# Performance work log

Measured on AMD Instinct MI355X. Metric: run time of the kernel, lower is better.

## Reference

```python
import jax, jax.numpy as jnp
import numpy as np

N = 50000   # nodes
E = 800000  # edges
F = 128     # feat_dim
LN_EPS = 1e-5


def setup_inputs() -> dict:
    key = jax.random.key(0)
    ks = jax.random.split(key, 16)

    def lin(k, fan_in, shape):
        # roughly kaiming-uniform-like scale; exact init is irrelevant for correctness
        return jax.random.normal(k, shape, jnp.float32) * (1.0 / np.sqrt(fan_in))

    inp = {
        "x": jax.random.normal(ks[0], (N, F), jnp.float32),
        "pos": jax.random.normal(ks[1], (N, 3), jnp.float32),
        "edge_index": jax.random.randint(ks[2], (2, E), 0, N, jnp.int64),
        # edge_mlp: Linear(2F+1 -> F), SiLU, Linear(F -> F)
        "ew1": lin(ks[3], 2 * F + 1, (2 * F + 1, F)),
        "eb1": jnp.zeros((F,), jnp.float32),
        "ew2": lin(ks[4], F, (F, F)),
        "eb2": jnp.zeros((F,), jnp.float32),
        # node_mlp: Linear(F -> F), SiLU, Linear(F -> F)
        "nw1": lin(ks[5], F, (F, F)),
        "nb1": jnp.zeros((F,), jnp.float32),
        "nw2": lin(ks[6], F, (F, F)),
        "nb2": jnp.zeros((F,), jnp.float32),
        # coord_mlp: Linear(F -> 1), Tanh
        "cw": lin(ks[7], F, (F, 1)),
        "cb": jnp.zeros((1,), jnp.float32),
        # LayerNorm(F)
        "gamma": jnp.ones((F,), jnp.float32),
        "beta": jnp.zeros((F,), jnp.float32),
    }
    return inp


def reference(x, pos, edge_index, ew1, eb1, ew2, eb2, nw1, nb1, nw2, nb2, cw, cb, gamma, beta):
    row, col = edge_index[0], edge_index[1]

    diff = pos[row] - pos[col]                              # [E, 3]
    dist2 = jnp.sum(diff * diff, axis=1, keepdims=True)     # [E, 1]
    edge_feat = jnp.concatenate([x[row], x[col], dist2], axis=1)  # [E, 2F+1]

    # edge MLP (dropout p=0 -> identity in eval)
    msg = jax.nn.silu(edge_feat @ ew1 + eb1) @ ew2 + eb2    # [E, F]

    # scatter-add messages to source nodes
    agg = jax.ops.segment_sum(msg, row, num_segments=N)     # [N, F]

    # node MLP + residual + LayerNorm
    upd = jax.nn.silu(agg @ nw1 + nb1) @ nw2 + nb2          # [N, F]
    pre = x + upd
    mean = jnp.mean(pre, axis=-1, keepdims=True)
    var = jnp.mean(jnp.square(pre - mean), axis=-1, keepdims=True)
    x_out = gamma * (pre - mean) * jax.lax.rsqrt(var + LN_EPS) + beta

    # coordinate update
    scale = jnp.tanh(msg @ cw + cb)                         # [E, 1]
    delta = jax.ops.segment_sum(scale * diff, row, num_segments=N)  # [N, 3]
    pos_out = pos + delta
    return (x_out, pos_out)
```

## Files before the change

### kernel.cpp

```cpp
#include <hip/hip_runtime.h>
#include <math.h>

#define NN 50000
#define EE 800000
#define FF 128

constexpr float LN_EPS = 1e-5f;
constexpr int NC = (NN + 255) / 256;

typedef float  f32x4  __attribute__((ext_vector_type(4)));
typedef short  s16x8  __attribute__((ext_vector_type(8)));
typedef unsigned short u16x4 __attribute__((ext_vector_type(4)));

__device__ __forceinline__ float silu_f(float v) {
    return v / (1.f + __expf(-v));
}

__device__ __forceinline__ unsigned short f2bf(float f) {
    union { float f; unsigned u; } cv; cv.f = f;
    unsigned u = cv.u;
    u += 0x7fffu + ((u >> 16) & 1u);
    return (unsigned short)(u >> 16);
}

__device__ __forceinline__ float bf2f(unsigned short u) {
    union { unsigned u; float f; } cv; cv.u = ((unsigned)u) << 16;
    return cv.f;
}

__global__ __launch_bounds__(256) void convert_x_kernel(
    const float* __restrict__ x, unsigned short* __restrict__ xb)
{
    int i = (blockIdx.x * 256 + threadIdx.x) * 8;
    float4 a = *(const float4*)&x[i];
    float4 b = *(const float4*)&x[i + 4];
    s16x8 o;
    o[0] = (short)f2bf(a.x); o[1] = (short)f2bf(a.y);
    o[2] = (short)f2bf(a.z); o[3] = (short)f2bf(a.w);
    o[4] = (short)f2bf(b.x); o[5] = (short)f2bf(b.y);
    o[6] = (short)f2bf(b.z); o[7] = (short)f2bf(b.w);
    *(s16x8*)&xb[i] = o;
}

__global__ __launch_bounds__(256) void transpose_w_kernel(
    const float* __restrict__ ew1, const float* __restrict__ ew2,
    const float* __restrict__ nw1, const float* __restrict__ nw2,
    unsigned short* __restrict__ ew1T, unsigned short* __restrict__ ew2T,
    unsigned short* __restrict__ nw1T, unsigned short* __restrict__ nw2T)
{
    int o = blockIdx.x * 256 + threadIdx.x;
    if (o < 32768) {
        int n = o >> 8, k = o & 255;
        ew1T[o] = f2bf(ew1[k * FF + n]);
    } else if (o < 49152) {
        int o2 = o - 32768; int n = o2 >> 7, k = o2 & 127;
        ew2T[o2] = f2bf(ew2[k * FF + n]);
    } else if (o < 65536) {
        int o2 = o - 49152; int n = o2 >> 7, k = o2 & 127;
        nw1T[o2] = f2bf(nw1[k * FF + n]);
    } else {
        int o2 = o - 65536; int n = o2 >> 7, k = o2 & 127;
        nw2T[o2] = f2bf(nw2[k * FF + n]);
    }
}

__global__ __launch_bounds__(256) void hist_kernel(
    const int* __restrict__ ei, int* __restrict__ cnt)
{
    int e = blockIdx.x * 256 + threadIdx.x;
    if (e < EE) atomicAdd(&cnt[ei[e]], 1);
}

__global__ __launch_bounds__(256) void chunk_sum_kernel(
    const int* __restrict__ cnt, int* __restrict__ chunkSum)
{
    __shared__ int s[256];
    int t = threadIdx.x;
    int idx = blockIdx.x * 256 + t;
    s[t] = (idx < NN) ? cnt[idx] : 0;
    __syncthreads();
    for (int off = 128; off > 0; off >>= 1) {
        if (t < off) s[t] += s[t + off];
        __syncthreads();
    }
    if (t == 0) chunkSum[blockIdx.x] = s[0];
}

__global__ __launch_bounds__(256) void scan_chunks_kernel(
    const int* __restrict__ chunkSum, int* __restrict__ chunkOff)
{
    __shared__ int s[256];
    int t = threadIdx.x;
    int v = (t < NC) ? chunkSum[t] : 0;
    s[t] = v;
    __syncthreads();
    for (int off = 1; off < 256; off <<= 1) {
        int u = (t >= off) ? s[t - off] : 0;
        __syncthreads();
        s[t] += u;
        __syncthreads();
    }
    if (t < NC) chunkOff[t] = s[t] - v;
}

__global__ __launch_bounds__(256) void scan_kernel(
    const int* __restrict__ cnt, const int* __restrict__ chunkOff,
    int* __restrict__ offs, int* __restrict__ rowStart)
{
    __shared__ int s[256];
    int t = threadIdx.x;
    int idx = blockIdx.x * 256 + t;
    int v = (idx < NN) ? cnt[idx] : 0;
    s[t] = v;
    __syncthreads();
    for (int off = 1; off < 256; off <<= 1) {
        int u = (t >= off) ? s[t - off] : 0;
        __syncthreads();
        s[t] += u;
        __syncthreads();
    }
    if (idx < NN) {
        int st = chunkOff[blockIdx.x] + s[t] - v;
        offs[idx] = st;
        rowStart[idx] = st;
    }
}

__global__ __launch_bounds__(256) void scatter_idx_kernel(
    const int* __restrict__ ei, int* __restrict__ offs,
    int* __restrict__ sRow, int* __restrict__ sCol)
{
    int e = blockIdx.x * 256 + threadIdx.x;
    if (e < EE) {
        int r = ei[e], c = ei[EE + e];
        int p = atomicAdd(&offs[r], 1);
        sRow[p] = r;
        sCol[p] = c;
    }
}

constexpr int EPB   = 64;
constexpr int NTILE = EE / EPB;
constexpr int XAS   = 264;
constexpr int H1S   = 136;

__global__ __launch_bounds__(512, 4) void edgeA_kernel(
    const unsigned short* __restrict__ xb, const float* __restrict__ pos,
    const int* __restrict__ sRow, const int* __restrict__ sCol,
    const unsigned short* __restrict__ ew1T, const float* __restrict__ ew1,
    const float* __restrict__ eb1,
    const unsigned short* __restrict__ ew2T, const float* __restrict__ eb2,
    const float* __restrict__ cw,  const float* __restrict__ cb,
    float* __restrict__ agg, float* __restrict__ sSg)
{
    __shared__ float dist2S[EPB];
    __shared__ int   rowS  [EPB];
    __shared__ float sPart[8][EPB];
    __shared__ __align__(16) unsigned short xa  [EPB * XAS];
    __shared__ __align__(16) unsigned short h1  [EPB * H1S];
    __shared__ __align__(16) unsigned short msgL[EPB * H1S];

    const int t   = threadIdx.x;
    const int w   = t >> 6;
    const int l   = t & 63;
    const int l15 = l & 15;
    const int q8  = l >> 4;
    const int n   = w * 16 + l15;

    s16x8 B1[8], B2[4];
    #pragma unroll
    for (int ko = 0; ko < 8; ++ko)
        B1[ko] = *(const s16x8*)(ew1T + (size_t)n * 256 + ko * 32 + q8 * 8);
    #pragma unroll
    for (int ko = 0; ko < 4; ++ko)
        B2[ko] = *(const s16x8*)(ew2T + (size_t)n * 128 + ko * 32 + q8 * 8);
    const float w256 = ew1[256 * FF + n];
    const float b1   = eb1[n];
    const float b2   = eb2[n];
    const float cwc  = cw[n];
    const float cb0  = cb[0];

    const int q   = t & 31;
    const int eB  = t >> 5;
    const int ksel = (q & 15) * 8;
    const int* idxBase = (q < 16) ? sRow : sCol;

    int   nidx[4];
    s16x8 ag[4];
    {
        int e0 = blockIdx.x * EPB;
        #pragma unroll
        for (int i = 0; i < 4; ++i) nidx[i] = idxBase[e0 + eB + 16 * i];
        #pragma unroll
        for (int i = 0; i < 4; ++i) ag[i] = *(const s16x8*)(xb + (size_t)nidx[i] * FF + ksel);
    }

    for (int tile = blockIdx.x; tile < NTILE; tile += gridDim.x) {
        const int e0 = tile * EPB;

        #pragma unroll
        for (int i = 0; i < 4; ++i)
            *(s16x8*)(xa + (eB + 16 * i) * XAS + q * 8) = ag[i];
        if (t < EPB) {
            int r = sRow[e0 + t];
            int c = sCol[e0 + t];
            rowS[t] = r;
            float dx = pos[r*3+0] - pos[c*3+0];
            float dy = pos[r*3+1] - pos[c*3+1];
            float dz = pos[r*3+2] - pos[c*3+2];
            dist2S[t] = dx*dx + dy*dy + dz*dz;
        }
        __syncthreads();

        {
            int tn  = tile + gridDim.x;
            int e0n = (tn < NTILE) ? tn * EPB : 0;
            #pragma unroll
            for (int i = 0; i < 4; ++i) nidx[i] = idxBase[e0n + eB + 16 * i];
            #pragma unroll
            for (int i = 0; i < 4; ++i) ag[i] = *(const s16x8*)(xb + (size_t)nidx[i] * FF + ksel);
        }

        f32x4 acc[4] = {};
        #pragma unroll
        for (int mt = 0; mt < 4; ++mt) {
            const unsigned short* ar = xa + (mt * 16 + l15) * XAS + q8 * 8;
            #pragma unroll
            for (int ko = 0; ko < 8; ++ko) {
                s16x8 a = *(const s16x8*)(ar + ko * 32);
                acc[mt] = __builtin_amdgcn_mfma_f32_16x16x32_bf16(a, B1[ko], acc[mt], 0, 0, 0);
            }
        }

        #pragma unroll
        for (int mt = 0; mt < 4; ++mt) {
            #pragma unroll
            for (int r = 0; r < 4; ++r) {
                int e = mt * 16 + q8 * 4 + r;
                float v = acc[mt][r] + dist2S[e] * w256 + b1;
                h1[e * H1S + n] = f2bf(silu_f(v));
            }
        }
        __syncthreads();

        f32x4 acc2[4] = {};
        #pragma unroll
        for (int mt = 0; mt < 4; ++mt) {
            const unsigned short* hr = h1 + (mt * 16 + l15) * H1S + q8 * 8;
            #pragma unroll
            for (int ko = 0; ko < 4; ++ko) {
                s16x8 a = *(const s16x8*)(hr + ko * 32);
                acc2[mt] = __builtin_amdgcn_mfma_f32_16x16x32_bf16(a, B2[ko], acc2[mt], 0, 0, 0);
            }
        }

        #pragma unroll
        for (int mt = 0; mt < 4; ++mt) {
            #pragma unroll
            for (int r = 0; r < 4; ++r) {
                float m = acc2[mt][r] + b2;
                float p = m * cwc;
                p += __shfl_xor(p, 1);
                p += __shfl_xor(p, 2);
                p += __shfl_xor(p, 4);
                p += __shfl_xor(p, 8);
                int e = mt * 16 + q8 * 4 + r;
                if (l15 == 0) sPart[w][e] = p;
                msgL[e * H1S + n] = f2bf(m);
            }
        }
        __syncthreads();

        if (t < EPB) {
            float p = 0.f;
            #pragma unroll
            for (int ww = 0; ww < 8; ++ww) p += sPart[ww][t];
            sSg[e0 + t] = tanhf(p + cb0);
        }

        {
            int c    = t & 127;
            int s    = t >> 7;
            int base = s * 16;
            float a  = 0.f;
            int cur  = rowS[base];
            #pragma unroll
            for (int k = 0; k < 16; ++k) {
                int e = base + k;
                int r = rowS[e];
                if (r != cur) {
                    atomicAdd(&agg[(size_t)cur * FF + c], a);
                    a = 0.f; cur = r;
                }
                a += bf2f(msgL[e * H1S + c]);
            }
            atomicAdd(&agg[(size_t)cur * FF + c], a);
        }
        __syncthreads();
    }
}

constexpr int NPB = 16;
constexpr int ABS = 136;

__global__ __launch_bounds__(512) void nodeB_kernel(
    const float* __restrict__ x, const float* __restrict__ pos,
    const float* __restrict__ agg, const float* __restrict__ sSg,
    const int* __restrict__ sCol, const int* __restrict__ rowStart,
    const unsigned short* __restrict__ nw1T, const float* __restrict__ nb1,
    const unsigned short* __restrict__ nw2T, const float* __restrict__ nb2,
    const float* __restrict__ gamma, const float* __restrict__ beta,
    float* __restrict__ xout, float* __restrict__ posout)
{
    __shared__ __align__(16) unsigned short aB [NPB * ABS];
    __shared__ __align__(16) unsigned short h1B[NPB * ABS];
    __shared__ float sRedS[8][NPB];
    __shared__ float sRedQ[8][NPB];
    __shared__ float sPosP[NPB][3][4];

    const int t   = threadIdx.x;
    const int w   = t >> 6;
    const int l   = t & 63;
    const int l15 = l & 15;
    const int q8  = l >> 4;
    const int n0  = blockIdx.x * NPB;
    const int n   = w * 16 + l15;

    {
        int idx = t * 4;
        int e = idx >> 7, c = idx & 127;
        float4 v = *(const float4*)&agg[(size_t)(n0 + e) * FF + c];
        u16x4 o;
        o[0] = f2bf(v.x); o[1] = f2bf(v.y); o[2] = f2bf(v.z); o[3] = f2bf(v.w);
        *(u16x4*)(aB + e * ABS + c) = o;
    }

    if (t < NPB * 12) {
        int e   = t / 12;
        int rem = t - e * 12;
        int d   = rem % 3;
        int ch  = rem / 3;
        int nn  = n0 + e;
        int p0  = rowStart[nn];
        int p1  = (nn == NN - 1) ? EE : rowStart[nn + 1];
        float pn = pos[nn * 3 + d];
        float sum = 0.f;
        for (int p = p0 + ch; p < p1; p += 4) {
            int c = sCol[p];
            sum += sSg[p] * (pn - pos[c * 3 + d]);
        }
        sPosP[e][d][ch] = sum;
    }
    __syncthreads();

    if (t < NPB * 3) {
        int e = t / 3, d = t % 3;
        int nn = n0 + e;
        posout[nn * 3 + d] = pos[nn * 3 + d]
            + sPosP[e][d][0] + sPosP[e][d][1] + sPosP[e][d][2] + sPosP[e][d][3];
    }

    f32x4 acc = {};
    {
        const unsigned short* ar = aB + l15 * ABS + q8 * 8;
        #pragma unroll
        for (int ko = 0; ko < 4; ++ko) {
            s16x8 a = *(const s16x8*)(ar + ko * 32);
            s16x8 b = *(const s16x8*)(nw1T + (size_t)n * 128 + ko * 32 + q8 * 8);
            acc = __builtin_amdgcn_mfma_f32_16x16x32_bf16(a, b, acc, 0, 0, 0);
        }
    }
    {
        float bb = nb1[n];
        #pragma unroll
        for (int r = 0; r < 4; ++r) {
            int e = q8 * 4 + r;
            h1B[e * ABS + n] = f2bf(silu_f(acc[r] + bb));
        }
    }
    __syncthreads();

    f32x4 acc2 = {};
    {
        const unsigned short* hr = h1B + l15 * ABS + q8 * 8;
        #pragma unroll
        for (int ko = 0; ko < 4; ++ko) {
            s16x8 a = *(const s16x8*)(hr + ko * 32);
            s16x8 b = *(const s16x8*)(nw2T + (size_t)n * 128 + ko * 32 + q8 * 8);
            acc2 = __builtin_amdgcn_mfma_f32_16x16x32_bf16(a, b, acc2, 0, 0, 0);
        }
    }

    float pre[4];
    {
        float bb = nb2[n];
        #pragma unroll
        for (int r = 0; r < 4; ++r) {
            int e = q8 * 4 + r;
            pre[r] = x[(size_t)(n0 + e) * FF + n] + acc2[r] + bb;
        }
    }
    #pragma unroll
    for (int r = 0; r < 4; ++r) {
        float s = pre[r], sq = pre[r] * pre[r];
        s += __shfl_xor(s, 1);  sq += __shfl_xor(sq, 1);
        s += __shfl_xor(s, 2);  sq += __shfl_xor(sq, 2);
        s += __shfl_xor(s, 4);  sq += __shfl_xor(sq, 4);
        s += __shfl_xor(s, 8);  sq += __shfl_xor(sq, 8);
        if (l15 == 0) {
            int e = q8 * 4 + r;
            sRedS[w][e] = s;
            sRedQ[w][e] = sq;
        }
    }
    __syncthreads();

    {
        float g = gamma[n], bt = beta[n];
        #pragma unroll
        for (int r = 0; r < 4; ++r) {
            int e = q8 * 4 + r;
            float S = 0.f, Q = 0.f;
            #pragma unroll
            for (int ww = 0; ww < 8; ++ww) { S += sRedS[ww][e]; Q += sRedQ[ww][e]; }
            float mean = S * (1.f / FF);
            float var  = Q * (1.f / FF) - mean * mean;
            xout[(size_t)(n0 + e) * FF + n] =
                g * (pre[r] - mean) * rsqrtf(var + LN_EPS) + bt;
        }
    }
}

extern "C" void kernel_launch(void* const* d_in, const int* in_sizes, int n_in,
                              void* d_out, int out_size, void* d_ws, size_t ws_size,
                              hipStream_t stream) {
    const float* x    = (const float*)d_in[0];
    const float* pos  = (const float*)d_in[1];
    const int*   ei   = (const int*)  d_in[2];
    const float* ew1  = (const float*)d_in[3];
    const float* eb1  = (const float*)d_in[4];
    const float* ew2  = (const float*)d_in[5];
    const float* eb2  = (const float*)d_in[6];
    const float* nw1  = (const float*)d_in[7];
    const float* nb1  = (const float*)d_in[8];
    const float* nw2  = (const float*)d_in[9];
    const float* nb2  = (const float*)d_in[10];
    const float* cw   = (const float*)d_in[11];
    const float* cb   = (const float*)d_in[12];
    const float* gam  = (const float*)d_in[13];
    const float* bet  = (const float*)d_in[14];

    float* out    = (float*)d_out;
    float* xout   = out;
    float* posout = out + (size_t)NN * FF;

    auto align256 = [](size_t v) { return (v + 255) & ~(size_t)255; };
    char* ws = (char*)d_ws;

    size_t CNT_B   = align256((size_t)NN * 4);
    size_t OFFS_B  = align256((size_t)NN * 4);
    size_t RST_B   = align256((size_t)NN * 4);
    size_t CHNK_B  = align256((size_t)NC * 4 * 2);
    size_t SROW_B  = align256((size_t)EE * 4);
    size_t XB_B    = align256((size_t)NN * FF * 2);
    size_t EW1T_B  = align256((size_t)128 * 256 * 2);
    size_t WT_B    = align256((size_t)128 * 128 * 2);
    size_t AGG_B   = align256((size_t)NN * FF * 4);

    size_t o = 0;
    int* cnt       = (int*)(ws + o);  o += CNT_B;
    int* offs      = (int*)(ws + o);  o += OFFS_B;
    int* rowStart  = (int*)(ws + o);  o += RST_B;
    int* chunkSum  = (int*)(ws + o);
    int* chunkOff  = chunkSum + NC;   o += CHNK_B;
    int* sRow      = (int*)(ws + o);  o += SROW_B;
    int* sCol      = (int*)(ws + o);  o += SROW_B;
    unsigned short* xb   = (unsigned short*)(ws + o);  o += XB_B;
    unsigned short* ew1T = (unsigned short*)(ws + o);  o += EW1T_B;
    unsigned short* ew2T = (unsigned short*)(ws + o);  o += WT_B;
    unsigned short* nw1T = (unsigned short*)(ws + o);  o += WT_B;
    unsigned short* nw2T = (unsigned short*)(ws + o);  o += WT_B;
    float*          agg  = (float*)(ws + o);           o += AGG_B;
    float*          sSg  = (float*)(ws + o);

    hipMemsetAsync(cnt, 0, CNT_B, stream);
    hipMemsetAsync(agg, 0, (size_t)NN * FF * 4, stream);

    convert_x_kernel<<<(NN * FF / 8) / 256, 256, 0, stream>>>(x, xb);
    transpose_w_kernel<<<(32768 + 3 * 16384) / 256, 256, 0, stream>>>(
        ew1, ew2, nw1, nw2, ew1T, ew2T, nw1T, nw2T);

    hist_kernel<<<(EE + 255) / 256, 256, 0, stream>>>(ei, cnt);
    chunk_sum_kernel<<<NC, 256, 0, stream>>>(cnt, chunkSum);
    scan_chunks_kernel<<<1, 256, 0, stream>>>(chunkSum, chunkOff);
    scan_kernel<<<NC, 256, 0, stream>>>(cnt, chunkOff, offs, rowStart);
    scatter_idx_kernel<<<(EE + 255) / 256, 256, 0, stream>>>(ei, offs, sRow, sCol);

    edgeA_kernel<<<2048, 512, 0, stream>>>(
        xb, pos, sRow, sCol, ew1T, ew1, eb1, ew2T, eb2, cw, cb, agg, sSg);

    nodeB_kernel<<<NN / NPB, 512, 0, stream>>>(
        x, pos, agg, sSg, sCol, rowStart,
        nw1T, nb1, nw2T, nb2, gam, bet, xout, posout);
}
```

Before: 503.1 us.

## Alias msg buffer onto xa, raise edge occupancy, parallelize coordinate reductions

The edge kernel reuses the xa shared buffer for bf16 messages instead of a separate msgL array. This cuts LDS per block, and the launch-bounds hint rises from 4 to 6 blocks per CU. The tanh coordinate-scale reduction now uses all threads with a transposed partial array and shuffles. The scatter now has each wave handle 8 edges with two channels per lane using 32-bit LDS loads. In the node kernel, the per-node position delta now uses 32 lanes per node with xyz together and a shuffle reduction, replacing 12 threads per node and an LDS stage. The higher occupancy target may squeeze registers, and aliasing xa assumes xa is dead by the time messages are written.

```diff
diff --git a/kernel.cpp b/kernel.cpp
--- a/kernel.cpp
+++ b/kernel.cpp
@@ -144,7 +144,7 @@
 constexpr int XAS   = 264;
 constexpr int H1S   = 136;
 
-__global__ __launch_bounds__(512, 4) void edgeA_kernel(
+__global__ __launch_bounds__(512, 6) void edgeA_kernel(
     const unsigned short* __restrict__ xb, const float* __restrict__ pos,
     const int* __restrict__ sRow, const int* __restrict__ sCol,
     const unsigned short* __restrict__ ew1T, const float* __restrict__ ew1,
@@ -155,10 +155,10 @@
 {
     __shared__ float dist2S[EPB];
     __shared__ int   rowS  [EPB];
-    __shared__ float sPart[8][EPB];
+    __shared__ float sPartT[EPB][8];
     __shared__ __align__(16) unsigned short xa  [EPB * XAS];
     __shared__ __align__(16) unsigned short h1  [EPB * H1S];
-    __shared__ __align__(16) unsigned short msgL[EPB * H1S];
+    unsigned short* msgL = xa;
 
     const int t   = threadIdx.x;
     const int w   = t >> 6;
@@ -265,36 +265,42 @@
                 p += __shfl_xor(p, 4);
                 p += __shfl_xor(p, 8);
                 int e = mt * 16 + q8 * 4 + r;
-                if (l15 == 0) sPart[w][e] = p;
+                if (l15 == 0) sPartT[e][w] = p;
                 msgL[e * H1S + n] = f2bf(m);
             }
         }
         __syncthreads();
 
-        if (t < EPB) {
-            float p = 0.f;
-            #pragma unroll
-            for (int ww = 0; ww < 8; ++ww) p += sPart[ww][t];
-            sSg[e0 + t] = tanhf(p + cb0);
-        }
-
         {
-            int c    = t & 127;
-            int s    = t >> 7;
-            int base = s * 16;
-            float a  = 0.f;
+            int e  = t >> 3;
+            int ww = t & 7;
+            float p = sPartT[e][ww];
+            p += __shfl_xor(p, 1);
+            p += __shfl_xor(p, 2);
+            p += __shfl_xor(p, 4);
+            if (ww == 0) sSg[e0 + e] = tanhf(p + cb0);
+        }
+
+        {
+            int c2   = l * 2;
+            int base = w * 8;
+            float a0 = 0.f, a1 = 0.f;
             int cur  = rowS[base];
             #pragma unroll
-            for (int k = 0; k < 16; ++k) {
+            for (int k = 0; k < 8; ++k) {
                 int e = base + k;
                 int r = rowS[e];
                 if (r != cur) {
-                    atomicAdd(&agg[(size_t)cur * FF + c], a);
-                    a = 0.f; cur = r;
+                    atomicAdd(&agg[(size_t)cur * FF + c2],     a0);
+                    atomicAdd(&agg[(size_t)cur * FF + c2 + 1], a1);
+                    a0 = 0.f; a1 = 0.f; cur = r;
                 }
-                a += bf2f(msgL[e * H1S + c]);
+                unsigned v = *(const unsigned*)(msgL + e * H1S + c2);
+                a0 += bf2f((unsigned short)(v & 0xffffu));
+                a1 += bf2f((unsigned short)(v >> 16));
             }
-            atomicAdd(&agg[(size_t)cur * FF + c], a);
+            atomicAdd(&agg[(size_t)cur * FF + c2],     a0);
+            atomicAdd(&agg[(size_t)cur * FF + c2 + 1], a1);
         }
         __syncthreads();
     }
@@ -316,7 +322,6 @@
     __shared__ __align__(16) unsigned short h1B[NPB * ABS];
     __shared__ float sRedS[8][NPB];
     __shared__ float sRedQ[8][NPB];
-    __shared__ float sPosP[NPB][3][4];
 
     const int t   = threadIdx.x;
     const int w   = t >> 6;
@@ -335,30 +340,34 @@
         *(u16x4*)(aB + e * ABS + c) = o;
     }
 
-    if (t < NPB * 12) {
-        int e   = t / 12;
-        int rem = t - e * 12;
-        int d   = rem % 3;
-        int ch  = rem / 3;
-        int nn  = n0 + e;
-        int p0  = rowStart[nn];
-        int p1  = (nn == NN - 1) ? EE : rowStart[nn + 1];
-        float pn = pos[nn * 3 + d];
-        float sum = 0.f;
-        for (int p = p0 + ch; p < p1; p += 4) {
+    {
+        int e  = t >> 5;
+        int ch = t & 31;
+        int nn = n0 + e;
+        int p0 = rowStart[nn];
+        int p1 = (nn == NN - 1) ? EE : rowStart[nn + 1];
+        float px = pos[nn*3+0], py = pos[nn*3+1], pz = pos[nn*3+2];
+        float sx = 0.f, sy = 0.f, sz = 0.f;
+        for (int p = p0 + ch; p < p1; p += 32) {
             int c = sCol[p];
-            sum += sSg[p] * (pn - pos[c * 3 + d]);
-        }
-        sPosP[e][d][ch] = sum;
+            float g = sSg[p];
+            sx += g * (px - pos[c*3+0]);
+            sy += g * (py - pos[c*3+1]);
+            sz += g * (pz - pos[c*3+2]);
+        }
+        #pragma unroll
+        for (int off = 1; off < 32; off <<= 1) {
+            sx += __shfl_xor(sx, off);
+            sy += __shfl_xor(sy, off);
+            sz += __shfl_xor(sz, off);
+        }
+        if (ch == 0) {
+            posout[nn*3+0] = px + sx;
+            posout[nn*3+1] = py + sy;
+            posout[nn*3+2] = pz + sz;
+        }
     }
     __syncthreads();
-
-    if (t < NPB * 3) {
-        int e = t / 3, d = t % 3;
-        int nn = n0 + e;
-        posout[nn * 3 + d] = pos[nn * 3 + d]
-            + sPosP[e][d][0] + sPosP[e][d][1] + sPosP[e][d][2] + sPosP[e][d][3];
-    }
 
     f32x4 acc = {};
     {
```

Result: slower. 605.8 us (+20.4%).
